# Optimization experiments

Measured on AMD Instinct MI355X. Metric: run time of the kernel, lower is better.

The kernel has to match this reference:

```python
import jax, jax.numpy as jnp
import numpy as np

E = 16        # n_routed_experts
TOP_K = 2
C = 768       # n_embd
I = 1536      # intermediate_size
B, T = 8, 2048


def setup_inputs() -> dict:
    key = jax.random.key(0)
    ks = jax.random.split(key, 9)
    s = 0.02  # init scale
    return {
        "x": jax.random.normal(ks[0], (B, T, C), jnp.float32),
        "w_gate": jax.random.normal(ks[1], (C, E), jnp.float32) * s,
        "expert_bias": jnp.zeros((E,), jnp.float32),
        "wg": jax.random.normal(ks[2], (E, C, I), jnp.float32) * s,
        "wu": jax.random.normal(ks[3], (E, C, I), jnp.float32) * s,
        "wd": jax.random.normal(ks[4], (E, I, C), jnp.float32) * s,
        "swg": jax.random.normal(ks[5], (C, I), jnp.float32) * s,
        "swu": jax.random.normal(ks[6], (C, I), jnp.float32) * s,
        "swd": jax.random.normal(ks[7], (I, C), jnp.float32) * s,
    }


def _expert(x, wg_e, wu_e, wd_e):
    # SwiGLU FFN: down(silu(gate(x)) * up(x))
    return (jax.nn.silu(x @ wg_e) * (x @ wu_e)) @ wd_e


def reference(x, w_gate, expert_bias, wg, wu, wd, swg, swu, swd):
    Bq, Tq, Cq = x.shape
    xf = x.reshape(-1, Cq)  # (N, C)
    n_tok = xf.shape[0]

    # shared experts (1 expert, divided by count=1)
    shared = _expert(xf, swg, swu, swd)

    # router: softmax over (logits + bias), top-k, renormalize
    logits = xf @ w_gate + expert_bias  # (N, E)
    probs = jax.nn.softmax(logits, axis=-1)
    topk_p, topk_i = jax.lax.top_k(probs, TOP_K)
    topk_p = topk_p / jnp.sum(topk_p, axis=-1, keepdims=True)

    # combine weights per expert: zero where expert not selected
    comb = jnp.zeros((n_tok, E), xf.dtype).at[
        jnp.arange(n_tok)[:, None], topk_i
    ].add(topk_p)  # (N, E)

    routed = jnp.zeros_like(xf)
    for e in range(E):  # fixed small expert count
        routed = routed + comb[:, e:e + 1] * _expert(xf, wg[e], wu[e], wd[e])

    return (shared + routed).reshape(Bq, Tq, Cq)
```

## Files before the change

kernel.cpp:

```cpp
#include <hip/hip_runtime.h>

typedef unsigned short u16;
typedef unsigned int u32;
typedef __attribute__((ext_vector_type(4))) float f32x4;
typedef __attribute__((ext_vector_type(8))) short short8;
typedef __attribute__((ext_vector_type(4))) u16 u16x4;
typedef __attribute__((ext_vector_type(8))) u16 u16x8;

#define N_TOK 16384
#define C_DIM 768
#define I_DIM 1536
#define N_EXP 16
#define TM 256
#define NT1 12
#define NT2 24
#define MAXT 208
#define PASS_T 104

#define CI_COUNTS 0
#define CI_STARTS 32
#define CI_NTILES 64
#define CI_TILE_E 128
#define CI_ESLOT 2048
#define CI_TOKW 36864
#define CI_PERM 102400
#define CI_RW 155648

#define XB_OFF  1048576u
#define WGU_OFF 26214400u
#define WDP_OFF 106430464u
#define ACT_OFF 146538496u

#define BAR() asm volatile("s_barrier" ::: "memory")
#define BAR_LG() asm volatile("s_waitcnt lgkmcnt(0)\n\ts_barrier" ::: "memory")
#define WAITVM(N) asm volatile("s_waitcnt vmcnt(" #N ")" ::: "memory")

__device__ __forceinline__ u16 f2bf(float f) {
  u32 x = __float_as_uint(f);
  return (u16)((x + 0x7FFFu + ((x >> 16) & 1u)) >> 16);
}
__device__ __forceinline__ float bf2f(u16 h) {
  return __uint_as_float(((u32)h) << 16);
}
__device__ __forceinline__ void dma16(const void* g, void* l) {
  __builtin_amdgcn_global_load_lds(
      (const __attribute__((address_space(1))) unsigned int*)g,
      (__attribute__((address_space(3))) unsigned int*)l, 16, 0, 0);
}

__global__ void convert_kernel(const float* __restrict__ wg, const float* __restrict__ wu,
                               const float* __restrict__ wd, const float* __restrict__ swg,
                               const float* __restrict__ swu, const float* __restrict__ swd,
                               u16* __restrict__ wgu, u16* __restrict__ wdp) {
  int bid = blockIdx.x;
  int tid = threadIdx.x, lane = tid & 63, wv = tid >> 6;
  int lsub = lane >> 3, lchk = lane & 7;
  if (bid < 17 * 96) {
    int e = bid / 96, nb = bid % 96;
    int ng = nb * 32 + wv * 8 + lsub;
    int gu = (ng >> 4) & 1;
    int scol = ((ng >> 5) << 4) | (ng & 15);
    const float* src = (e < N_EXP) ? ((gu ? wu : wg) + (size_t)e * C_DIM * I_DIM)
                                   : (gu ? swu : swg);
    u16* drow = wgu + ((size_t)e * (2 * I_DIM) + ng) * C_DIM;
    const float* s0 = src + scol;
    for (int k0 = 0; k0 < C_DIM; k0 += 64) {
      u16x8 o;
#pragma unroll
      for (int j = 0; j < 8; j++) o[j] = f2bf(s0[(size_t)(k0 + lchk * 8 + j) * I_DIM]);
      *(u16x8*)&drow[k0 + lchk * 8] = o;
    }
  } else {
    int b2 = bid - 17 * 96;
    int e = b2 / 24, nb = b2 % 24;
    const float* src = (e < N_EXP) ? (wd + (size_t)e * I_DIM * C_DIM) : swd;
    u16* dst = wdp + (size_t)e * (I_DIM * C_DIM);
    int ng = nb * 32 + wv * 8 + lsub;
    const float* s0 = src + ng;
    u16* drow = dst + (size_t)ng * I_DIM;
    for (int k0 = 0; k0 < I_DIM; k0 += 64) {
      u16x8 o;
#pragma unroll
      for (int j = 0; j < 8; j++) o[j] = f2bf(s0[(size_t)(k0 + lchk * 8 + j) * C_DIM]);
      *(u16x8*)&drow[k0 + lchk * 8] = o;
    }
  }
}

__global__ void router_kernel(const float* __restrict__ x, const float* __restrict__ wgate,
                              const float* __restrict__ ebias, int* __restrict__ ctrl,
                              u16* __restrict__ xb) {
  __shared__ float xs[16 * 772];
  __shared__ float wgsT[16 * 772];
  __shared__ float lg[16 * 16];
  int tid = threadIdx.x;
  int tok0 = blockIdx.x * 16;
  const float4* xsrc = (const float4*)(x + (size_t)tok0 * C_DIM);
  const float4* wsrc = (const float4*)wgate;
#pragma unroll
  for (int j = 0; j < 12; j++) {
    int q = tid + j * 256;
    float4 v = xsrc[q];
    int tk = q / 192;
    int c4 = q - tk * 192;
    *(float4*)&xs[tk * 772 + c4 * 4] = v;
    u16x4 o; o.x = f2bf(v.x); o.y = f2bf(v.y); o.z = f2bf(v.z); o.w = f2bf(v.w);
    *(u16x4*)(xb + (size_t)tok0 * C_DIM + (size_t)q * 4) = o;
    float4 w = wsrc[q];
    int c = q >> 2, e0 = (q & 3) * 4;
    wgsT[(e0 + 0) * 772 + c] = w.x;
    wgsT[(e0 + 1) * 772 + c] = w.y;
    wgsT[(e0 + 2) * 772 + c] = w.z;
    wgsT[(e0 + 3) * 772 + c] = w.w;
  }
  __syncthreads();
  int tk = tid >> 4, e = tid & 15;
  float acc = ebias[e];
  const float4* xr = (const float4*)&xs[tk * 772];
  const float4* wr = (const float4*)&wgsT[e * 772];
#pragma unroll 4
  for (int c4 = 0; c4 < 192; c4++) {
    float4 xv = xr[c4], wv = wr[c4];
    acc = fmaf(xv.x, wv.x, fmaf(xv.y, wv.y, fmaf(xv.z, wv.z, fmaf(xv.w, wv.w, acc))));
  }
  lg[tk * 16 + e] = acc;
  __syncthreads();
  if (tid < 16) {
    int n = tok0 + tid;
    float l0 = -1e30f, l1 = -1e30f; int i0 = 0, i1 = 0;
#pragma unroll
    for (int j = 0; j < 16; j++) {
      float l = lg[tid * 16 + j];
      if (l > l0) { l1 = l0; i1 = i0; l0 = l; i0 = j; }
      else if (l > l1) { l1 = l; i1 = j; }
    }
    float e1 = __expf(l1 - l0);
    float inv = 1.f / (1.f + e1);
    int s0 = atomicAdd(&ctrl[CI_COUNTS + i0], 1);
    int s1 = atomicAdd(&ctrl[CI_COUNTS + i1], 1);
    ctrl[CI_ESLOT + 2 * n]     = (i0 << 24) | s0;
    ctrl[CI_ESLOT + 2 * n + 1] = (i1 << 24) | s1;
    float* tw = (float*)(ctrl + CI_TOKW);
    tw[2 * n] = inv; tw[2 * n + 1] = e1 * inv;
  }
}

__global__ void tiles_kernel(int* __restrict__ ctrl) {
  if (threadIdx.x != 0) return;
  int cnt[17];
#pragma unroll
  for (int e = 0; e < 16; e++) cnt[e] = ctrl[CI_COUNTS + e];
  cnt[16] = N_TOK;
  ctrl[CI_COUNTS + 16] = N_TOK;
  int cur = 0, T = 0;
  for (int e = 0; e <= 16; e++) {
    ctrl[CI_STARTS + e] = cur;
    int nt = (cnt[e] + TM - 1) >> 8;
    for (int i = 0; i < nt; i++) ctrl[CI_TILE_E + T++] = e;
    cur += nt << 8;
  }
  ctrl[CI_NTILES] = T;
}

__global__ void scatter_kernel(int* __restrict__ ctrl) {
  int n = blockIdx.x * 256 + threadIdx.x;
  const float* tw = (const float*)(ctrl + CI_TOKW);
  float* rw = (float*)(ctrl + CI_RW);
#pragma unroll
  for (int k = 0; k < 2; k++) {
    int es = ctrl[CI_ESLOT + 2 * n + k];
    int e = es >> 24;
    int slot = es & 0xFFFFFF;
    int row = ctrl[CI_STARTS + e] + slot;
    ctrl[CI_PERM + row] = n;
    rw[row] = tw[2 * n + k];
  }
  int srow = ctrl[CI_STARTS + 16] + n;
  ctrl[CI_PERM + srow] = n;
  rw[srow] = 1.0f;
}

__global__ __launch_bounds__(512, 2)
void gemm1_kernel(const u16* __restrict__ xb, const u16* __restrict__ wgu,
                  u16* __restrict__ act, const int* __restrict__ ctrl, int tile0) {
  __shared__ u16 As[2][2][8192];
  __shared__ u16 Bs[2][2][8192];
  int tt = tile0 + blockIdx.x;
  if (tt >= ctrl[CI_NTILES]) return;
  int e = ctrl[CI_TILE_E + tt];
  int row0 = tt << 8;
  int row0l = blockIdx.x << 8;
  int col0c = blockIdx.y << 8;
  int seg = ctrl[CI_STARTS + e];
  bool sh = (e == N_EXP);
  const u16* W = wgu + (size_t)e * (2 * I_DIM * C_DIM);
  int rlim = sh ? 0x7fffffff : (seg + ctrl[CI_COUNTS + e]);
  const int* perm = ctrl + CI_PERM;
  int tid = threadIdx.x, lane = tid & 63, wv = tid >> 6;
  int lr = lane & 15, lq = lane >> 4;
  int kcl = (lane & 3) ^ ((lane >> 2) & 3);
  const u16 *aS0, *aS1, *bS0, *bS1;
  {
    int r0 = row0 + wv * 16 + (lane >> 2);
    int r1 = r0 + 128;
    int t0 = sh ? (r0 - seg) : ((r0 < rlim) ? perm[r0] : 0);
    int t1 = sh ? (r1 - seg) : ((r1 < rlim) ? perm[r1] : 0);
    aS0 = xb + (size_t)t0 * C_DIM + kcl * 8;
    aS1 = xb + (size_t)t1 * C_DIM + kcl * 8;
    int cb = col0c + wv * 16 + (lane >> 2);
    bS0 = W + (size_t)cb * C_DIM + kcl * 8;
    bS1 = W + (size_t)(cb + 128) * C_DIM + kcl * 8;
  }
  int dofs = tid * 8;

  auto stA = [&](int kt, int kh) {
    u16* d = &As[kt & 1][kh][dofs];
    int ko = kt * 64 + kh * 32;
    dma16(aS0 + ko, d);
    dma16(aS1 + ko, d + 4096);
  };
  auto stB = [&](int kt, int kh) {
    u16* d = &Bs[kt & 1][kh][dofs];
    int ko = kt * 64 + kh * 32;
    dma16(bS0 + ko, d);
    dma16(bS1 + ko, d + 4096);
  };

  f32x4 acc[8][4];
#pragma unroll
  for (int m = 0; m < 8; m++)
#pragma unroll
    for (int n = 0; n < 4; n++) {
      f32x4 z = {0.f, 0.f, 0.f, 0.f};
      acc[m][n] = z;
    }
  int wr = wv >> 2, wc = wv & 3;
  short8 afr[4], bfr[4];

  auto rdB = [&](int s, int kh) {
#pragma unroll
    for (int n = 0; n < 4; n++) {
      int i = wc * 64 + n * 16 + lr;
      bfr[n] = *(const short8*)&Bs[s][kh][i * 32 + ((lq ^ (i & 3)) * 8)];
    }
  };
  auto rdA = [&](int s, int kh, int g) {
#pragma unroll
    for (int m = 0; m < 4; m++) {
      int r = wr * 128 + g * 64 + m * 16 + lr;
      afr[m] = *(const short8*)&As[s][kh][r * 32 + ((lq ^ (r & 3)) * 8)];
    }
  };
  auto mm = [&](int g) {
    __builtin_amdgcn_s_setprio(1);
#pragma unroll
    for (int m = 0; m < 4; m++)
#pragma unroll
      for (int n = 0; n < 4; n++)
        acc[g * 4 + m][n] = __builtin_amdgcn_mfma_f32_16x16x32_bf16(
            afr[m], bfr[n], acc[g * 4 + m][n], 0, 0, 0);
    __builtin_amdgcn_s_setprio(0);
  };

  stA(0, 0); stB(0, 0); stA(0, 1); stB(0, 1); stA(1, 0); stB(1, 0);
  WAITVM(8);
  BAR();
  for (int kt = 0; kt < NT1; ++kt) {
    int s = kt & 1;
    rdB(s, 0); rdA(s, 0, 0);
    if (kt + 1 < NT1) stA(kt + 1, 1);
    BAR(); mm(0); BAR_LG();
    rdA(s, 0, 1);
    if (kt + 1 < NT1) stB(kt + 1, 1);
    if (kt == NT1 - 1) { WAITVM(0); } else { WAITVM(8); }
    BAR(); mm(1); BAR_LG();
    rdB(s, 1); rdA(s, 1, 0);
    if (kt + 2 < NT1) stA(kt + 2, 0);
    BAR(); mm(0); BAR_LG();
    rdA(s, 1, 1);
    if (kt + 2 < NT1) stB(kt + 2, 0);
    if (kt < NT1 - 2) { WAITVM(8); } else if (kt == NT1 - 2) { WAITVM(4); }
    BAR(); mm(1); BAR_LG();
  }
  int cbase = (blockIdx.y << 7) + wc * 32;
#pragma unroll
  for (int mi = 0; mi < 8; mi++)
#pragma unroll
    for (int np = 0; np < 2; np++)
#pragma unroll
      for (int rg = 0; rg < 4; rg++) {
        float g = acc[mi][2 * np][rg];
        float h = acc[mi][2 * np + 1][rg];
        float a = g * (1.f / (1.f + __expf(-g))) * h;
        int r_loc = wr * 128 + mi * 16 + lq * 4 + rg;
        act[(size_t)(row0l + r_loc) * I_DIM + cbase + np * 16 + lr] = f2bf(a);
      }
}

__global__ __launch_bounds__(256, 2)
void gemm2_kernel(const u16* __restrict__ act, const u16* __restrict__ wdp,
                  float* __restrict__ out, const int* __restrict__ ctrl, int tile0) {
  __shared__ u16 As[2][2][4096];
  __shared__ u16 Bs[2][2][4096];
  int bx = blockIdx.x;
  int tt = tile0 + (bx >> 1);
  if (tt >= ctrl[CI_NTILES]) return;
  int e = ctrl[CI_TILE_E + tt];
  int sub = bx & 1;
  int row0g = (tt << 8) + (sub << 7);
  int row0l = bx << 7;
  int col0 = blockIdx.y << 7;
  const u16* D = wdp + (size_t)e * (I_DIM * C_DIM);
  int tid = threadIdx.x, lane = tid & 63, wv = tid >> 6;
  int lr = lane & 15, lq = lane >> 4;
  int kcl = (tid & 3) ^ ((tid >> 2) & 3);
  const u16 *aS0, *aS1, *bS0, *bS1;
  {
    int r0 = tid >> 2;
    aS0 = act + (size_t)(row0l + r0) * I_DIM + kcl * 8;
    aS1 = act + (size_t)(row0l + r0 + 64) * I_DIM + kcl * 8;
    bS0 = D + (size_t)(col0 + r0) * I_DIM + kcl * 8;
    bS1 = D + (size_t)(col0 + r0 + 64) * I_DIM + kcl * 8;
  }
  int dofs = tid * 8;

  auto stA = [&](int kt, int kh) {
    u16* d = &As[kt & 1][kh][dofs];
    int ko = kt * 64 + kh * 32;
    dma16(aS0 + ko, d);
    dma16(aS1 + ko, d + 2048);
  };
  auto stB = [&](int kt, int kh) {
    u16* d = &Bs[kt & 1][kh][dofs];
    int ko = kt * 64 + kh * 32;
    dma16(bS0 + ko, d);
    dma16(bS1 + ko, d + 2048);
  };

  f32x4 acc[4][4];
#pragma unroll
  for (int m = 0; m < 4; m++)
#pragma unroll
    for (int n = 0; n < 4; n++) {
      f32x4 z = {0.f, 0.f, 0.f, 0.f};
      acc[m][n] = z;
    }
  int wr = wv >> 1, wc = wv & 1;
  short8 afr[4], bfr[4];

  auto rdB = [&](int s, int kh) {
#pragma unroll
    for (int n = 0; n < 4; n++) {
      int i = wc * 64 + n * 16 + lr;
      bfr[n] = *(const short8*)&Bs[s][kh][i * 32 + ((lq ^ (i & 3)) * 8)];
    }
  };
  auto rdA = [&](int s, int kh) {
#pragma unroll
    for (int m = 0; m < 4; m++) {
      int r = wr * 64 + m * 16 + lr;
      afr[m] = *(const short8*)&As[s][kh][r * 32 + ((lq ^ (r & 3)) * 8)];
    }
  };
  auto mm = [&]() {
    __builtin_amdgcn_s_setprio(1);
#pragma unroll
    for (int m = 0; m < 4; m++)
#pragma unroll
      for (int n = 0; n < 4; n++)
        acc[m][n] = __builtin_amdgcn_mfma_f32_16x16x32_bf16(afr[m], bfr[n], acc[m][n], 0, 0, 0);
    __builtin_amdgcn_s_setprio(0);
  };

  stA(0, 0); stB(0, 0); stA(0, 1); stB(0, 1); stA(1, 0); stB(1, 0);
  WAITVM(8);
  BAR();
  for (int kt = 0; kt < NT2; ++kt) {
    int s = kt & 1;
    rdB(s, 0); rdA(s, 0);
    if (kt + 1 < NT2) { stA(kt + 1, 1); stB(kt + 1, 1); }
    if (kt == NT2 - 1) { WAITVM(0); } else { WAITVM(8); }
    BAR(); mm(); BAR_LG();
    rdB(s, 1); rdA(s, 1);
    if (kt + 2 < NT2) { stA(kt + 2, 0); stB(kt + 2, 0); }
    if (kt < NT2 - 2) { WAITVM(8); } else if (kt == NT2 - 2) { WAITVM(4); }
    BAR(); mm(); BAR_LG();
  }
  const int* perm = ctrl + CI_PERM;
  const float* rw = (const float*)(ctrl + CI_RW);
#pragma unroll
  for (int m = 0; m < 4; m++)
#pragma unroll
    for (int rg = 0; rg < 4; rg++) {
      int rgrow = row0g + wr * 64 + m * 16 + lq * 4 + rg;
      int tokn = perm[rgrow];
      if (tokn < 0) continue;
      float w = rw[rgrow];
      float* obase = out + (size_t)tokn * C_DIM + col0 + wc * 64 + lr;
#pragma unroll
      for (int n = 0; n < 4; n++)
        atomicAdd(obase + n * 16, acc[m][n][rg] * w);
    }
}

extern "C" void kernel_launch(void* const* d_in, const int* in_sizes, int n_in,
                              void* d_out, int out_size, void* d_ws, size_t ws_size,
                              hipStream_t stream) {
  (void)in_sizes; (void)n_in; (void)out_size; (void)ws_size;
  const float* x     = (const float*)d_in[0];
  const float* wgate = (const float*)d_in[1];
  const float* ebias = (const float*)d_in[2];
  const float* wg    = (const float*)d_in[3];
  const float* wu    = (const float*)d_in[4];
  const float* wd    = (const float*)d_in[5];
  const float* swg   = (const float*)d_in[6];
  const float* swu   = (const float*)d_in[7];
  const float* swd   = (const float*)d_in[8];
  float* out = (float*)d_out;
  char* ws = (char*)d_ws;
  int* ctrl = (int*)ws;
  u16* xb  = (u16*)(ws + XB_OFF);
  u16* wgu = (u16*)(ws + WGU_OFF);
  u16* wdp = (u16*)(ws + WDP_OFF);
  u16* act = (u16*)(ws + ACT_OFF);

  hipMemsetAsync(ws, 0, 256, stream);
  hipMemsetAsync(ws + (size_t)CI_PERM * 4, 0xFF, 53248 * 4, stream);
  hipMemsetAsync(d_out, 0, (size_t)N_TOK * C_DIM * 4, stream);
  router_kernel<<<N_TOK / 16, 256, 0, stream>>>(x, wgate, ebias, ctrl, xb);
  tiles_kernel<<<1, 64, 0, stream>>>(ctrl);
  scatter_kernel<<<N_TOK / 256, 256, 0, stream>>>(ctrl);
  convert_kernel<<<17 * 96 + 17 * 24, 256, 0, stream>>>(wg, wu, wd, swg, swu, swd, wgu, wdp);
  for (int p = 0; p < 2; p++) {
    gemm1_kernel<<<dim3(PASS_T, 2 * I_DIM / 256), 512, 0, stream>>>(xb, wgu, act, ctrl, p * PASS_T);
    gemm2_kernel<<<dim3(2 * PASS_T, C_DIM / 128), 256, 0, stream>>>(act, wdp, out, ctrl, p * PASS_T);
  }
}
```

Before: 1.078 ms.

## Load full 64-wide K rows per lane with 8-chunk XOR swizzle and finer prefetch schedule

Both GEMM kernels now stage each K-tile as contiguous 64-element rows (128 bytes per row across 8 lanes) instead of two 32-wide halves, using an 8-way XOR swizzle for LDS bank spreading. The intent is more coalesced global loads, with full cache lines fetched per row. The prefetch schedule is reworked so the next tile's loads are spread across four MFMA phases. gemm2 also splits its A-fragment reads into halves to interleave with MMA. The lgkmcnt waits before barriers are dropped, which relies on the compiler inserting LDS waits and risks subtle ordering issues.

```diff
diff --git a/kernel.cpp b/kernel.cpp
--- a/kernel.cpp
+++ b/kernel.cpp
@@ -12,6 +12,7 @@
 #define I_DIM 1536
 #define N_EXP 16
 #define TM 256
+#define BK 64
 #define NT1 12
 #define NT2 24
 #define MAXT 208
@@ -32,7 +33,6 @@
 #define ACT_OFF 146538496u
 
 #define BAR() asm volatile("s_barrier" ::: "memory")
-#define BAR_LG() asm volatile("s_waitcnt lgkmcnt(0)\n\ts_barrier" ::: "memory")
 #define WAITVM(N) asm volatile("s_waitcnt vmcnt(" #N ")" ::: "memory")
 
 __device__ __forceinline__ u16 f2bf(float f) {
@@ -183,8 +183,8 @@
 __global__ __launch_bounds__(512, 2)
 void gemm1_kernel(const u16* __restrict__ xb, const u16* __restrict__ wgu,
                   u16* __restrict__ act, const int* __restrict__ ctrl, int tile0) {
-  __shared__ u16 As[2][2][8192];
-  __shared__ u16 Bs[2][2][8192];
+  __shared__ u16 As[2][256 * 64];
+  __shared__ u16 Bs[2][256 * 64];
   int tt = tile0 + blockIdx.x;
   if (tt >= ctrl[CI_NTILES]) return;
   int e = ctrl[CI_TILE_E + tt];
@@ -197,34 +197,20 @@
   int rlim = sh ? 0x7fffffff : (seg + ctrl[CI_COUNTS + e]);
   const int* perm = ctrl + CI_PERM;
   int tid = threadIdx.x, lane = tid & 63, wv = tid >> 6;
-  int lr = lane & 15, lq = lane >> 4;
-  int kcl = (lane & 3) ^ ((lane >> 2) & 3);
-  const u16 *aS0, *aS1, *bS0, *bS1;
-  {
-    int r0 = row0 + wv * 16 + (lane >> 2);
-    int r1 = r0 + 128;
-    int t0 = sh ? (r0 - seg) : ((r0 < rlim) ? perm[r0] : 0);
-    int t1 = sh ? (r1 - seg) : ((r1 < rlim) ? perm[r1] : 0);
-    aS0 = xb + (size_t)t0 * C_DIM + kcl * 8;
-    aS1 = xb + (size_t)t1 * C_DIM + kcl * 8;
-    int cb = col0c + wv * 16 + (lane >> 2);
-    bS0 = W + (size_t)cb * C_DIM + kcl * 8;
-    bS1 = W + (size_t)(cb + 128) * C_DIM + kcl * 8;
-  }
-  int dofs = tid * 8;
-
-  auto stA = [&](int kt, int kh) {
-    u16* d = &As[kt & 1][kh][dofs];
-    int ko = kt * 64 + kh * 32;
-    dma16(aS0 + ko, d);
-    dma16(aS1 + ko, d + 4096);
-  };
-  auto stB = [&](int kt, int kh) {
-    u16* d = &Bs[kt & 1][kh][dofs];
-    int ko = kt * 64 + kh * 32;
-    dma16(bS0 + ko, d);
-    dma16(bS1 + ko, d + 4096);
-  };
+  int lsub = lane >> 3, lchk = lane & 7;
+  int co = (lchk ^ lsub) * 8;
+  const u16 *aS[4], *bS[4];
+#pragma unroll
+  for (int h = 0; h < 4; h++) {
+    int r = row0 + h * 64 + wv * 8 + lsub;
+    int tok = sh ? (r - seg) : ((r < rlim) ? perm[r] : 0);
+    aS[h] = xb + (size_t)tok * C_DIM + co;
+    bS[h] = W + (size_t)(col0c + h * 64 + wv * 8 + lsub) * C_DIM + co;
+  }
+  int dbase = wv * 512;
+
+  auto stA = [&](int kt, int h) { dma16(aS[h] + kt * BK, &As[kt & 1][h * 4096 + dbase]); };
+  auto stB = [&](int kt, int h) { dma16(bS[h] + kt * BK, &Bs[kt & 1][h * 4096 + dbase]); };
 
   f32x4 acc[8][4];
 #pragma unroll
@@ -234,6 +220,7 @@
       f32x4 z = {0.f, 0.f, 0.f, 0.f};
       acc[m][n] = z;
     }
+  int lr = lane & 15, lq = lane >> 4;
   int wr = wv >> 2, wc = wv & 3;
   short8 afr[4], bfr[4];
 
@@ -241,14 +228,14 @@
 #pragma unroll
     for (int n = 0; n < 4; n++) {
       int i = wc * 64 + n * 16 + lr;
-      bfr[n] = *(const short8*)&Bs[s][kh][i * 32 + ((lq ^ (i & 3)) * 8)];
+      bfr[n] = *(const short8*)&Bs[s][i * 64 + (((kh * 4 + lq) ^ (i & 7)) * 8)];
     }
   };
   auto rdA = [&](int s, int kh, int g) {
 #pragma unroll
     for (int m = 0; m < 4; m++) {
       int r = wr * 128 + g * 64 + m * 16 + lr;
-      afr[m] = *(const short8*)&As[s][kh][r * 32 + ((lq ^ (r & 3)) * 8)];
+      afr[m] = *(const short8*)&As[s][r * 64 + (((kh * 4 + lq) ^ (r & 7)) * 8)];
     }
   };
   auto mm = [&](int g) {
@@ -262,25 +249,26 @@
     __builtin_amdgcn_s_setprio(0);
   };
 
-  stA(0, 0); stB(0, 0); stA(0, 1); stB(0, 1); stA(1, 0); stB(1, 0);
-  WAITVM(8);
+#pragma unroll
+  for (int h = 0; h < 4; h++) { stA(0, h); stB(0, h); }
+  stA(1, 0); stA(1, 2);
+  WAITVM(2);
   BAR();
   for (int kt = 0; kt < NT1; ++kt) {
     int s = kt & 1;
     rdB(s, 0); rdA(s, 0, 0);
-    if (kt + 1 < NT1) stA(kt + 1, 1);
-    BAR(); mm(0); BAR_LG();
+    if (kt + 1 < NT1) { stA(kt + 1, 1); stB(kt + 1, 0); }
+    BAR(); mm(0); BAR();
     rdA(s, 0, 1);
-    if (kt + 1 < NT1) stB(kt + 1, 1);
-    if (kt == NT1 - 1) { WAITVM(0); } else { WAITVM(8); }
-    BAR(); mm(1); BAR_LG();
+    if (kt + 1 < NT1) { stA(kt + 1, 3); stB(kt + 1, 1); }
+    BAR(); mm(1); BAR();
     rdB(s, 1); rdA(s, 1, 0);
-    if (kt + 2 < NT1) stA(kt + 2, 0);
-    BAR(); mm(0); BAR_LG();
+    if (kt + 1 < NT1) { stB(kt + 1, 2); stB(kt + 1, 3); }
+    BAR(); mm(0); BAR();
     rdA(s, 1, 1);
-    if (kt + 2 < NT1) stB(kt + 2, 0);
-    if (kt < NT1 - 2) { WAITVM(8); } else if (kt == NT1 - 2) { WAITVM(4); }
-    BAR(); mm(1); BAR_LG();
+    if (kt + 2 < NT1) { stA(kt + 2, 0); stA(kt + 2, 2); WAITVM(2); }
+    else if (kt + 1 < NT1) { WAITVM(0); }
+    BAR(); mm(1); BAR();
   }
   int cbase = (blockIdx.y << 7) + wc * 32;
 #pragma unroll
@@ -300,8 +288,8 @@
 __global__ __launch_bounds__(256, 2)
 void gemm2_kernel(const u16* __restrict__ act, const u16* __restrict__ wdp,
                   float* __restrict__ out, const int* __restrict__ ctrl, int tile0) {
-  __shared__ u16 As[2][2][4096];
-  __shared__ u16 Bs[2][2][4096];
+  __shared__ u16 As[2][128 * 64];
+  __shared__ u16 Bs[2][128 * 64];
   int bx = blockIdx.x;
   int tt = tile0 + (bx >> 1);
   if (tt >= ctrl[CI_NTILES]) return;
@@ -312,30 +300,18 @@
   int col0 = blockIdx.y << 7;
   const u16* D = wdp + (size_t)e * (I_DIM * C_DIM);
   int tid = threadIdx.x, lane = tid & 63, wv = tid >> 6;
-  int lr = lane & 15, lq = lane >> 4;
-  int kcl = (tid & 3) ^ ((tid >> 2) & 3);
-  const u16 *aS0, *aS1, *bS0, *bS1;
-  {
-    int r0 = tid >> 2;
-    aS0 = act + (size_t)(row0l + r0) * I_DIM + kcl * 8;
-    aS1 = act + (size_t)(row0l + r0 + 64) * I_DIM + kcl * 8;
-    bS0 = D + (size_t)(col0 + r0) * I_DIM + kcl * 8;
-    bS1 = D + (size_t)(col0 + r0 + 64) * I_DIM + kcl * 8;
-  }
-  int dofs = tid * 8;
-
-  auto stA = [&](int kt, int kh) {
-    u16* d = &As[kt & 1][kh][dofs];
-    int ko = kt * 64 + kh * 32;
-    dma16(aS0 + ko, d);
-    dma16(aS1 + ko, d + 2048);
-  };
-  auto stB = [&](int kt, int kh) {
-    u16* d = &Bs[kt & 1][kh][dofs];
-    int ko = kt * 64 + kh * 32;
-    dma16(bS0 + ko, d);
-    dma16(bS1 + ko, d + 2048);
-  };
+  int lsub = lane >> 3, lchk = lane & 7;
+  int co = (lchk ^ lsub) * 8;
+  const u16 *aS[4], *bS[4];
+#pragma unroll
+  for (int q = 0; q < 4; q++) {
+    aS[q] = act + (size_t)(row0l + q * 32 + wv * 8 + lsub) * I_DIM + co;
+    bS[q] = D + (size_t)(col0 + q * 32 + wv * 8 + lsub) * I_DIM + co;
+  }
+  int dbase = wv * 512;
+
+  auto stA = [&](int kt, int q) { dma16(aS[q] + kt * BK, &As[kt & 1][q * 2048 + dbase]); };
+  auto stB = [&](int kt, int q) { dma16(bS[q] + kt * BK, &Bs[kt & 1][q * 2048 + dbase]); };
 
   f32x4 acc[4][4];
 #pragma unroll
@@ -345,61 +321,70 @@
       f32x4 z = {0.f, 0.f, 0.f, 0.f};
       acc[m][n] = z;
     }
+  int lr = lane & 15, lq = lane >> 4;
   int wr = wv >> 1, wc = wv & 1;
-  short8 afr[4], bfr[4];
+  short8 afr[2], bfr[4];
 
   auto rdB = [&](int s, int kh) {
 #pragma unroll
     for (int n = 0; n < 4; n++) {
       int i = wc * 64 + n * 16 + lr;
-      bfr[n] = *(const short8*)&Bs[s][kh][i * 32 + ((lq ^ (i & 3)) * 8)];
-    }
-  };
-  auto rdA = [&](int s, int kh) {
-#pragma unroll
-    for (int m = 0; m < 4; m++) {
-      int r = wr * 64 + m * 16 + lr;
-      afr[m] = *(const short8*)&As[s][kh][r * 32 + ((lq ^ (r & 3)) * 8)];
-    }
-  };
-  auto mm = [&]() {
+      bfr[n] = *(const short8*)&Bs[s][i * 64 + (((kh * 4 + lq) ^ (i & 7)) * 8)];
+    }
+  };
+  auto rdA = [&](int s, int kh, int mh) {
+#pragma unroll
+    for (int m = 0; m < 2; m++) {
+      int r = wr * 64 + mh * 32 + m * 16 + lr;
+      afr[m] = *(const short8*)&As[s][r * 64 + (((kh * 4 + lq) ^ (r & 7)) * 8)];
+    }
+  };
+  auto mm = [&](int mh) {
     __builtin_amdgcn_s_setprio(1);
 #pragma unroll
-    for (int m = 0; m < 4; m++)
+    for (int m = 0; m < 2; m++)
 #pragma unroll
       for (int n = 0; n < 4; n++)
-        acc[m][n] = __builtin_amdgcn_mfma_f32_16x16x32_bf16(afr[m], bfr[n], acc[m][n], 0, 0, 0);
+        acc[mh * 2 + m][n] = __builtin_amdgcn_mfma_f32_16x16x32_bf16(
+            afr[m], bfr[n], acc[mh * 2 + m][n], 0, 0, 0);
     __builtin_amdgcn_s_setprio(0);
   };
 
-  stA(0, 0); stB(0, 0); stA(0, 1); stB(0, 1); stA(1, 0); stB(1, 0);
-  WAITVM(8);
+#pragma unroll
+  for (int q = 0; q < 4; q++) { stA(0, q); stB(0, q); }
+  stA(1, 0); stA(1, 2);
+  WAITVM(2);
   BAR();
   for (int kt = 0; kt < NT2; ++kt) {
     int s = kt & 1;
-    rdB(s, 0); rdA(s, 0);
-    if (kt + 1 < NT2) { stA(kt + 1, 1); stB(kt + 1, 1); }
-    if (kt == NT2 - 1) { WAITVM(0); } else { WAITVM(8); }
-    BAR(); mm(); BAR_LG();
-    rdB(s, 1); rdA(s, 1);
-    if (kt + 2 < NT2) { stA(kt + 2, 0); stB(kt + 2, 0); }
-    if (kt < NT2 - 2) { WAITVM(8); } else if (kt == NT2 - 2) { WAITVM(4); }
-    BAR(); mm(); BAR_LG();
+    rdB(s, 0); rdA(s, 0, 0);
+    if (kt + 1 < NT2) { stA(kt + 1, 1); stB(kt + 1, 0); }
+    BAR(); mm(0); BAR();
+    rdA(s, 0, 1);
+    if (kt + 1 < NT2) { stA(kt + 1, 3); stB(kt + 1, 1); }
+    BAR(); mm(1); BAR();
+    rdB(s, 1); rdA(s, 1, 0);
+    if (kt + 1 < NT2) { stB(kt + 1, 2); stB(kt + 1, 3); }
+    BAR(); mm(0); BAR();
+    rdA(s, 1, 1);
+    if (kt + 2 < NT2) { stA(kt + 2, 0); stA(kt + 2, 2); WAITVM(2); }
+    else if (kt + 1 < NT2) { WAITVM(0); }
+    BAR(); mm(1); BAR();
   }
   const int* perm = ctrl + CI_PERM;
   const float* rw = (const float*)(ctrl + CI_RW);
 #pragma unroll
-  for (int m = 0; m < 4; m++)
+  for (int mi = 0; mi < 4; mi++)
 #pragma unroll
     for (int rg = 0; rg < 4; rg++) {
-      int rgrow = row0g + wr * 64 + m * 16 + lq * 4 + rg;
+      int rgrow = row0g + wr * 64 + mi * 16 + lq * 4 + rg;
       int tokn = perm[rgrow];
       if (tokn < 0) continue;
       float w = rw[rgrow];
       float* obase = out + (size_t)tokn * C_DIM + col0 + wc * 64 + lr;
 #pragma unroll
       for (int n = 0; n < 4; n++)
-        atomicAdd(obase + n * 16, acc[m][n][rg] * w);
+        atomicAdd(obase + n * 16, acc[mi][n][rg] * w);
     }
 }
 
```

New measurement: 1.126 ms. +4.5%, slower.
